# Performance work log

Hardware: AMD Instinct MI355X
Metric: run time of the kernel (lower is better)

The kernel has to match this reference:

```python
import jax, jax.numpy as jnp
import numpy as np

B, T1, T2, D = 16, 64, 64, 1024
PROJ = D // 2


def setup_inputs() -> dict:
    key = jax.random.key(0)
    k1, k2, k3 = jax.random.split(key, 3)
    x = jax.random.normal(k1, (B, T1, T2, D), dtype=jnp.float32)
    # glorot-style scale for params
    W_proj = jax.random.normal(k2, (D, PROJ), dtype=jnp.float32) * (2.0 / (D + PROJ)) ** 0.5
    v_score = jax.random.normal(k3, (PROJ,), dtype=jnp.float32) * (1.0 / PROJ) ** 0.5
    return {"x": x, "W_proj": W_proj, "v_score": v_score}


def reference(x, W_proj, v_score):
    # proj_input = tanh(tensordot(x, W_proj, axes=(3,0)))  -> (B, T1, T2, PROJ)
    proj = jnp.tanh(jnp.einsum('btsd,dp->btsp', x, W_proj))
    # att_scores = tensordot(proj, v_score, axes=(3,0))    -> (B, T1, T2)
    scores = jnp.einsum('btsp,p->bts', proj, v_score)
    # softmax over last axis (T2), weighted sum of x over T2 -> (B, T1, D)
    attn = jax.nn.softmax(scores, axis=-1)
    out = jnp.einsum('bts,btsd->btd', attn, x)
    return out
```

## Files before the change

kernel.cpp:

```cpp
#include <hip/hip_runtime.h>
#include <hip/hip_bf16.h>
#include <math.h>

#define B_    16
#define T1_   64
#define T2_   64
#define D_    1024
#define PROJ_ 512
#define BM    64
#define BK    32
#define NT    (D_ / BK)
#define LDP   40

typedef __attribute__((ext_vector_type(8))) short bf16x8;
typedef __attribute__((ext_vector_type(4))) float f32x4;
typedef __attribute__((ext_vector_type(4))) unsigned int u32x4;

__device__ __forceinline__ unsigned short f2bf(float f) {
  unsigned int u = __builtin_bit_cast(unsigned int, f);
  u += 0x7FFFu + ((u >> 16) & 1u);
  return (unsigned short)(u >> 16);
}

__device__ __forceinline__ float fast_tanh(float a) {
  float t = __builtin_amdgcn_exp2f(a * 2.885390081777927f);
  return 1.0f - 2.0f * __builtin_amdgcn_rcpf(t + 1.0f);
}

__global__ __launch_bounds__(256) void make_bfrag(
    const float* __restrict__ W, unsigned short* __restrict__ wt) {
  __shared__ float tile[32][33];
  const int t  = blockIdx.x;
  const int np = blockIdx.y;
  const int tx = threadIdx.x & 31;
  const int ty = threadIdx.x >> 5;
#pragma unroll
  for (int i = 0; i < 4; ++i)
    tile[ty + i * 8][tx] =
        W[(size_t)(t * 32 + ty + i * 8) * PROJ_ + np * 32 + tx];
  __syncthreads();
  if (threadIdx.x < 128) {
    const int sub  = threadIdx.x >> 6;
    const int lane = threadIdx.x & 63;
    const int llo = lane & 15, lhi = lane >> 4;
    unsigned short o[8];
#pragma unroll
    for (int j = 0; j < 8; ++j)
      o[j] = f2bf(tile[lhi * 8 + j][sub * 16 + llo]);
    const int n16 = np * 2 + sub;
    *(u32x4*)(wt + ((size_t)(t * 32 + n16) * 64 + lane) * 8) = *(const u32x4*)o;
  }
}

__global__ __launch_bounds__(512, 4) void fused_kernel(
    const float* __restrict__ x, const unsigned short* __restrict__ wt,
    const float* __restrict__ v, float* __restrict__ out) {
  __shared__ unsigned short As[2][BM][LDP];
  __shared__ float sp[BM][9];
  __shared__ float attn[BM];
  __shared__ f32x4 xred[256];

  const int tid  = threadIdx.x;
  const int lane = tid & 63;
  const int wid  = tid >> 6;
  const int llo  = lane & 15, lhi = lane >> 4;
  const int bt   = blockIdx.x;
  const int m0   = bt * BM;

  f32x4 acc[4][4];
#pragma unroll
  for (int mf = 0; mf < 4; ++mf)
#pragma unroll
    for (int nf = 0; nf < 4; ++nf) acc[mf][nf] = (f32x4){0.f, 0.f, 0.f, 0.f};

  const int arow = tid >> 3, akc = (tid & 7) * 4;
  const float* asrc = x + (size_t)(m0 + arow) * D_ + akc;

  const u32x4* wt4 = (const u32x4*)wt;
  const int bbase = (wid * 4) * 64 + lane;

  float4 s0 = *(const float4*)(asrc);
  float4 s1 = *(const float4*)(asrc + BK);
  u32x4 rb[4];
#pragma unroll
  for (int nf = 0; nf < 4; ++nf) rb[nf] = wt4[bbase + nf * 64];
  {
    ushort4 ua = {f2bf(s0.x), f2bf(s0.y), f2bf(s0.z), f2bf(s0.w)};
    *(ushort4*)&As[0][arow][akc] = ua;
  }
  asm volatile("s_waitcnt lgkmcnt(0)" ::: "memory");
  __builtin_amdgcn_s_barrier();

#define KSTEP(T, SLD, SCV, BR, BW)                                           \
  {                                                                          \
    bf16x8 af0 = *(const bf16x8*)&As[BR][ 0 + llo][lhi * 8];                 \
    bf16x8 af1 = *(const bf16x8*)&As[BR][16 + llo][lhi * 8];                 \
    bf16x8 af2 = *(const bf16x8*)&As[BR][32 + llo][lhi * 8];                 \
    bf16x8 af3 = *(const bf16x8*)&As[BR][48 + llo][lhi * 8];                 \
    if ((T) + 2 < NT) SLD = *(const float4*)(asrc + ((T) + 2) * BK);         \
    _Pragma("unroll")                                                        \
    for (int nf = 0; nf < 4; ++nf) {                                         \
      bf16x8 bfr = *(const bf16x8*)&rb[nf];                                  \
      acc[0][nf] = __builtin_amdgcn_mfma_f32_16x16x32_bf16(af0, bfr, acc[0][nf], 0, 0, 0); \
      acc[1][nf] = __builtin_amdgcn_mfma_f32_16x16x32_bf16(af1, bfr, acc[1][nf], 0, 0, 0); \
      acc[2][nf] = __builtin_amdgcn_mfma_f32_16x16x32_bf16(af2, bfr, acc[2][nf], 0, 0, 0); \
      acc[3][nf] = __builtin_amdgcn_mfma_f32_16x16x32_bf16(af3, bfr, acc[3][nf], 0, 0, 0); \
      if ((T) + 1 < NT) rb[nf] = wt4[bbase + ((T) + 1) * 2048 + nf * 64];    \
    }                                                                        \
    if ((T) + 1 < NT) {                                                      \
      ushort4 ua = {f2bf(SCV.x), f2bf(SCV.y), f2bf(SCV.z), f2bf(SCV.w)};     \
      *(ushort4*)&As[BW][arow][akc] = ua;                                    \
    }                                                                        \
    asm volatile("s_waitcnt lgkmcnt(0)" ::: "memory");                       \
    __builtin_amdgcn_s_barrier();                                            \
  }

  for (int t = 0; t < NT; t += 2) {
    KSTEP(t,     s0, s1, 0, 1)
    KSTEP(t + 1, s1, s0, 1, 0)
  }
#undef KSTEP

  float vv0 = v[wid * 64 +  0 + llo];
  float vv1 = v[wid * 64 + 16 + llo];
  float vv2 = v[wid * 64 + 32 + llo];
  float vv3 = v[wid * 64 + 48 + llo];
#pragma unroll
  for (int mf = 0; mf < 4; ++mf) {
    float pr[4] = {0.f, 0.f, 0.f, 0.f};
#pragma unroll
    for (int r = 0; r < 4; ++r) {
      pr[r] += fast_tanh(acc[mf][0][r]) * vv0;
      pr[r] += fast_tanh(acc[mf][1][r]) * vv1;
      pr[r] += fast_tanh(acc[mf][2][r]) * vv2;
      pr[r] += fast_tanh(acc[mf][3][r]) * vv3;
    }
#pragma unroll
    for (int r = 0; r < 4; ++r) {
      float p = pr[r];
      p += __shfl_xor(p, 1, 64);
      p += __shfl_xor(p, 2, 64);
      p += __shfl_xor(p, 4, 64);
      p += __shfl_xor(p, 8, 64);
      if (llo == 0) sp[mf * 16 + lhi * 4 + r][wid] = p;
    }
  }
  __syncthreads();

  if (tid < BM) {
    float s = 0.f;
#pragma unroll
    for (int w = 0; w < 8; ++w) s += sp[tid][w];
    float mx = s;
#pragma unroll
    for (int mask = 1; mask < 64; mask <<= 1)
      mx = fmaxf(mx, __shfl_xor(mx, mask, 64));
    const float e = __builtin_amdgcn_exp2f((s - mx) * 1.442695040888963f);
    float sum = e;
#pragma unroll
    for (int mask = 1; mask < 64; mask <<= 1)
      sum += __shfl_xor(sum, mask, 64);
    attn[tid] = e * __builtin_amdgcn_rcpf(sum);
  }
  __syncthreads();

  const int c4 = tid & 255;
  const int sh = tid >> 8;
  const float* xg = x + ((size_t)m0 + sh * 32) * D_ + c4 * 4;
  f32x4 o0 = {0.f,0.f,0.f,0.f}, o1 = o0, o2 = o0, o3 = o0;
#pragma unroll
  for (int s = 0; s < 32; s += 4) {
    const float w0 = attn[sh * 32 + s + 0];
    const float w1 = attn[sh * 32 + s + 1];
    const float w2 = attn[sh * 32 + s + 2];
    const float w3 = attn[sh * 32 + s + 3];
    const float4 a0 = *(const float4*)(xg + (size_t)(s + 0) * D_);
    const float4 a1 = *(const float4*)(xg + (size_t)(s + 1) * D_);
    const float4 a2 = *(const float4*)(xg + (size_t)(s + 2) * D_);
    const float4 a3 = *(const float4*)(xg + (size_t)(s + 3) * D_);
    o0[0] += w0 * a0.x; o0[1] += w0 * a0.y; o0[2] += w0 * a0.z; o0[3] += w0 * a0.w;
    o1[0] += w1 * a1.x; o1[1] += w1 * a1.y; o1[2] += w1 * a1.z; o1[3] += w1 * a1.w;
    o2[0] += w2 * a2.x; o2[1] += w2 * a2.y; o2[2] += w2 * a2.z; o2[3] += w2 * a2.w;
    o3[0] += w3 * a3.x; o3[1] += w3 * a3.y; o3[2] += w3 * a3.z; o3[3] += w3 * a3.w;
  }
  f32x4 o;
#pragma unroll
  for (int j = 0; j < 4; ++j) o[j] = (o0[j] + o1[j]) + (o2[j] + o3[j]);
  if (sh == 1) xred[c4] = o;
  __syncthreads();
  if (sh == 0) {
    f32x4 o2b = xred[c4];
    float4 res = {o[0] + o2b[0], o[1] + o2b[1], o[2] + o2b[2], o[3] + o2b[3]};
    *(float4*)(out + (size_t)bt * D_ + c4 * 4) = res;
  }
}

extern "C" void kernel_launch(void* const* d_in, const int* in_sizes, int n_in,
                              void* d_out, int out_size, void* d_ws, size_t ws_size,
                              hipStream_t stream) {
  const float* x = (const float*)d_in[0];
  const float* W = (const float*)d_in[1];
  const float* v = (const float*)d_in[2];
  float* out = (float*)d_out;
  unsigned short* Wt = (unsigned short*)d_ws;

  make_bfrag<<<dim3(NT, PROJ_ / 32), 256, 0, stream>>>(W, Wt);
  fused_kernel<<<B_ * T1_, 512, 0, stream>>>(x, Wt, v, out);
}
```

Before: 118.9 us.

## Stage weight fragments through LDS via direct global-to-LDS loads

Replaces per-wave register prefetch of the bf16 weight fragments with global_load_lds DMA into a double-buffered LDS region, which each wave then reads back for its MFMA B operand. This is meant to cut register pressure and let the hardware write loaded data straight to LDS, overlapping the next tile's fetch with compute. In exchange it uses about 74KB of LDS per block, which limits how many 512-thread blocks fit per CU. It also adds a full vmcnt(0) wait before every barrier, which stalls on the x prefetch as well.

```diff
diff --git a/kernel.cpp b/kernel.cpp
--- a/kernel.cpp
+++ b/kernel.cpp
@@ -27,6 +27,12 @@
   return 1.0f - 2.0f * __builtin_amdgcn_rcpf(t + 1.0f);
 }
 
+__device__ __forceinline__ void load_lds16(const void* g, void* l) {
+  __builtin_amdgcn_global_load_lds(
+      (const __attribute__((address_space(1))) unsigned int*)g,
+      (__attribute__((address_space(3))) unsigned int*)l, 16, 0, 0);
+}
+
 __global__ __launch_bounds__(256) void make_bfrag(
     const float* __restrict__ W, unsigned short* __restrict__ wt) {
   __shared__ float tile[32][33];
@@ -55,10 +61,14 @@
 __global__ __launch_bounds__(512, 4) void fused_kernel(
     const float* __restrict__ x, const unsigned short* __restrict__ wt,
     const float* __restrict__ v, float* __restrict__ out) {
-  __shared__ unsigned short As[2][BM][LDP];
-  __shared__ float sp[BM][9];
-  __shared__ float attn[BM];
-  __shared__ f32x4 xred[256];
+  __shared__ __align__(16) char smem[75776];
+  unsigned short (*As)[BM][LDP] = (unsigned short(*)[BM][LDP])smem;
+  unsigned short* Bs0 = (unsigned short*)(smem + 10240);
+  unsigned short* Bs1 = Bs0 + 16384;
+#define BSP(i) ((i) ? Bs1 : Bs0)
+  float (*sp)[9] = (float(*)[9])smem;
+  float* attn    = (float*)(smem + 2304);
+  f32x4* xred    = (f32x4*)(smem + 2560);
 
   const int tid  = threadIdx.x;
   const int lane = tid & 63;
@@ -75,43 +85,50 @@
 
   const int arow = tid >> 3, akc = (tid & 7) * 4;
   const float* asrc = x + (size_t)(m0 + arow) * D_ + akc;
-
   const u32x4* wt4 = (const u32x4*)wt;
-  const int bbase = (wid * 4) * 64 + lane;
 
   float4 s0 = *(const float4*)(asrc);
   float4 s1 = *(const float4*)(asrc + BK);
-  u32x4 rb[4];
-#pragma unroll
-  for (int nf = 0; nf < 4; ++nf) rb[nf] = wt4[bbase + nf * 64];
   {
     ushort4 ua = {f2bf(s0.x), f2bf(s0.y), f2bf(s0.z), f2bf(s0.w)};
     *(ushort4*)&As[0][arow][akc] = ua;
   }
-  asm volatile("s_waitcnt lgkmcnt(0)" ::: "memory");
+#pragma unroll
+  for (int c = 0; c < 4; ++c) {
+    const int n16 = c * 8 + wid;
+    load_lds16(wt4 + (size_t)n16 * 64 + lane, Bs0 + n16 * 512);
+  }
+  asm volatile("s_waitcnt vmcnt(0) lgkmcnt(0)" ::: "memory");
   __builtin_amdgcn_s_barrier();
 
 #define KSTEP(T, SLD, SCV, BR, BW)                                           \
   {                                                                          \
+    if ((T) + 1 < NT) {                                                      \
+      _Pragma("unroll")                                                      \
+      for (int c = 0; c < 4; ++c) {                                          \
+        const int n16 = c * 8 + wid;                                         \
+        load_lds16(wt4 + (size_t)(((T) + 1) * 32 + n16) * 64 + lane,         \
+                   BSP(BW) + n16 * 512);                                     \
+      }                                                                      \
+    }                                                                        \
+    if ((T) + 2 < NT) SLD = *(const float4*)(asrc + ((T) + 2) * BK);         \
     bf16x8 af0 = *(const bf16x8*)&As[BR][ 0 + llo][lhi * 8];                 \
     bf16x8 af1 = *(const bf16x8*)&As[BR][16 + llo][lhi * 8];                 \
     bf16x8 af2 = *(const bf16x8*)&As[BR][32 + llo][lhi * 8];                 \
     bf16x8 af3 = *(const bf16x8*)&As[BR][48 + llo][lhi * 8];                 \
-    if ((T) + 2 < NT) SLD = *(const float4*)(asrc + ((T) + 2) * BK);         \
     _Pragma("unroll")                                                        \
     for (int nf = 0; nf < 4; ++nf) {                                         \
-      bf16x8 bfr = *(const bf16x8*)&rb[nf];                                  \
+      bf16x8 bfr = *(const bf16x8*)(BSP(BR) + ((wid * 4 + nf) * 64 + lane) * 8); \
       acc[0][nf] = __builtin_amdgcn_mfma_f32_16x16x32_bf16(af0, bfr, acc[0][nf], 0, 0, 0); \
       acc[1][nf] = __builtin_amdgcn_mfma_f32_16x16x32_bf16(af1, bfr, acc[1][nf], 0, 0, 0); \
       acc[2][nf] = __builtin_amdgcn_mfma_f32_16x16x32_bf16(af2, bfr, acc[2][nf], 0, 0, 0); \
       acc[3][nf] = __builtin_amdgcn_mfma_f32_16x16x32_bf16(af3, bfr, acc[3][nf], 0, 0, 0); \
-      if ((T) + 1 < NT) rb[nf] = wt4[bbase + ((T) + 1) * 2048 + nf * 64];    \
     }                                                                        \
     if ((T) + 1 < NT) {                                                      \
       ushort4 ua = {f2bf(SCV.x), f2bf(SCV.y), f2bf(SCV.z), f2bf(SCV.w)};     \
       *(ushort4*)&As[BW][arow][akc] = ua;                                    \
     }                                                                        \
-    asm volatile("s_waitcnt lgkmcnt(0)" ::: "memory");                       \
+    asm volatile("s_waitcnt vmcnt(0) lgkmcnt(0)" ::: "memory");              \
     __builtin_amdgcn_s_barrier();                                            \
   }
 
@@ -120,6 +137,7 @@
     KSTEP(t + 1, s1, s0, 1, 0)
   }
 #undef KSTEP
+#undef BSP
 
   float vv0 = v[wid * 64 +  0 + llo];
   float vv1 = v[wid * 64 + 16 + llo];
```

Result: slower. 122.5 us (+3.1%).

## Halve block size, loop each wave over two projection slices

Applied to the files above, without the earlier changes.

Shrinks the fused block from 8 waves to 4 and has each wave compute two PROJ slices in sequential passes, restaging the x tile each pass with wider 8-element loads. Adds s_setprio around the MFMA burst and simplifies the final weighted sum so each thread reduces all 64 rows, removing the shared-memory cross-half reduction. The goal is better occupancy and less barrier overhead, at the cost of re-reading and reconverting the x tile twice per block.

```diff
diff --git a/kernel.cpp b/kernel.cpp
--- a/kernel.cpp
+++ b/kernel.cpp
@@ -10,11 +10,14 @@
 #define BM    64
 #define BK    32
 #define NT    (D_ / BK)
+#define NPASS 2
 #define LDP   40
 
 typedef __attribute__((ext_vector_type(8))) short bf16x8;
 typedef __attribute__((ext_vector_type(4))) float f32x4;
 typedef __attribute__((ext_vector_type(4))) unsigned int u32x4;
+
+struct A8 { float4 a, b; };
 
 __device__ __forceinline__ unsigned short f2bf(float f) {
   unsigned int u = __builtin_bit_cast(unsigned int, f);
@@ -52,13 +55,12 @@
   }
 }
 
-__global__ __launch_bounds__(512, 4) void fused_kernel(
+__global__ __launch_bounds__(256, 4) void fused_kernel(
     const float* __restrict__ x, const unsigned short* __restrict__ wt,
     const float* __restrict__ v, float* __restrict__ out) {
   __shared__ unsigned short As[2][BM][LDP];
-  __shared__ float sp[BM][9];
+  __shared__ float sp[BM][8];
   __shared__ float attn[BM];
-  __shared__ f32x4 xred[256];
 
   const int tid  = threadIdx.x;
   const int lane = tid & 63;
@@ -67,29 +69,37 @@
   const int bt   = blockIdx.x;
   const int m0   = bt * BM;
 
-  f32x4 acc[4][4];
-#pragma unroll
-  for (int mf = 0; mf < 4; ++mf)
-#pragma unroll
-    for (int nf = 0; nf < 4; ++nf) acc[mf][nf] = (f32x4){0.f, 0.f, 0.f, 0.f};
-
-  const int arow = tid >> 3, akc = (tid & 7) * 4;
+  const int arow = tid >> 2, akc = (tid & 3) * 8;
   const float* asrc = x + (size_t)(m0 + arow) * D_ + akc;
-
   const u32x4* wt4 = (const u32x4*)wt;
-  const int bbase = (wid * 4) * 64 + lane;
-
-  float4 s0 = *(const float4*)(asrc);
-  float4 s1 = *(const float4*)(asrc + BK);
-  u32x4 rb[4];
-#pragma unroll
-  for (int nf = 0; nf < 4; ++nf) rb[nf] = wt4[bbase + nf * 64];
-  {
-    ushort4 ua = {f2bf(s0.x), f2bf(s0.y), f2bf(s0.z), f2bf(s0.w)};
-    *(ushort4*)&As[0][arow][akc] = ua;
-  }
-  asm volatile("s_waitcnt lgkmcnt(0)" ::: "memory");
-  __builtin_amdgcn_s_barrier();
+
+  for (int p = 0; p < NPASS; ++p) {
+    const int slice = p * 4 + wid;
+    const int bbase = (slice * 4) * 64 + lane;
+
+    f32x4 acc[4][4];
+#pragma unroll
+    for (int mf = 0; mf < 4; ++mf)
+#pragma unroll
+      for (int nf = 0; nf < 4; ++nf) acc[mf][nf] = (f32x4){0.f, 0.f, 0.f, 0.f};
+
+    __syncthreads();
+
+    A8 s0, s1;
+    s0.a = *(const float4*)(asrc);
+    s0.b = *(const float4*)(asrc + 4);
+    s1.a = *(const float4*)(asrc + BK);
+    s1.b = *(const float4*)(asrc + BK + 4);
+    u32x4 rb[4];
+#pragma unroll
+    for (int nf = 0; nf < 4; ++nf) rb[nf] = wt4[bbase + nf * 64];
+    {
+      unsigned short o[8] = {f2bf(s0.a.x), f2bf(s0.a.y), f2bf(s0.a.z), f2bf(s0.a.w),
+                             f2bf(s0.b.x), f2bf(s0.b.y), f2bf(s0.b.z), f2bf(s0.b.w)};
+      *(u32x4*)&As[0][arow][akc] = *(const u32x4*)o;
+    }
+    asm volatile("s_waitcnt lgkmcnt(0)" ::: "memory");
+    __builtin_amdgcn_s_barrier();
 
 #define KSTEP(T, SLD, SCV, BR, BW)                                           \
   {                                                                          \
@@ -97,7 +107,11 @@
     bf16x8 af1 = *(const bf16x8*)&As[BR][16 + llo][lhi * 8];                 \
     bf16x8 af2 = *(const bf16x8*)&As[BR][32 + llo][lhi * 8];                 \
     bf16x8 af3 = *(const bf16x8*)&As[BR][48 + llo][lhi * 8];                 \
-    if ((T) + 2 < NT) SLD = *(const float4*)(asrc + ((T) + 2) * BK);         \
+    if ((T) + 2 < NT) {                                                      \
+      SLD.a = *(const float4*)(asrc + ((T) + 2) * BK);                       \
+      SLD.b = *(const float4*)(asrc + ((T) + 2) * BK + 4);                   \
+    }                                                                        \
+    __builtin_amdgcn_s_setprio(1);                                           \
     _Pragma("unroll")                                                        \
     for (int nf = 0; nf < 4; ++nf) {                                         \
       bf16x8 bfr = *(const bf16x8*)&rb[nf];                                  \
@@ -107,42 +121,47 @@
       acc[3][nf] = __builtin_amdgcn_mfma_f32_16x16x32_bf16(af3, bfr, acc[3][nf], 0, 0, 0); \
       if ((T) + 1 < NT) rb[nf] = wt4[bbase + ((T) + 1) * 2048 + nf * 64];    \
     }                                                                        \
+    __builtin_amdgcn_s_setprio(0);                                           \
     if ((T) + 1 < NT) {                                                      \
-      ushort4 ua = {f2bf(SCV.x), f2bf(SCV.y), f2bf(SCV.z), f2bf(SCV.w)};     \
-      *(ushort4*)&As[BW][arow][akc] = ua;                                    \
+      unsigned short o[8] = {f2bf(SCV.a.x), f2bf(SCV.a.y), f2bf(SCV.a.z), f2bf(SCV.a.w), \
+                             f2bf(SCV.b.x), f2bf(SCV.b.y), f2bf(SCV.b.z), f2bf(SCV.b.w)}; \
+      *(u32x4*)&As[BW][arow][akc] = *(const u32x4*)o;                        \
     }                                                                        \
     asm volatile("s_waitcnt lgkmcnt(0)" ::: "memory");                       \
     __builtin_amdgcn_s_barrier();                                            \
   }
 
-  for (int t = 0; t < NT; t += 2) {
-    KSTEP(t,     s0, s1, 0, 1)
-    KSTEP(t + 1, s1, s0, 1, 0)
-  }
+    for (int t = 0; t < NT; t += 2) {
+      KSTEP(t,     s0, s1, 0, 1)
+      KSTEP(t + 1, s1, s0, 1, 0)
+    }
 #undef KSTEP
 
-  float vv0 = v[wid * 64 +  0 + llo];
-  float vv1 = v[wid * 64 + 16 + llo];
-  float vv2 = v[wid * 64 + 32 + llo];
-  float vv3 = v[wid * 64 + 48 + llo];
-#pragma unroll
-  for (int mf = 0; mf < 4; ++mf) {
-    float pr[4] = {0.f, 0.f, 0.f, 0.f};
-#pragma unroll
-    for (int r = 0; r < 4; ++r) {
-      pr[r] += fast_tanh(acc[mf][0][r]) * vv0;
-      pr[r] += fast_tanh(acc[mf][1][r]) * vv1;
-      pr[r] += fast_tanh(acc[mf][2][r]) * vv2;
-      pr[r] += fast_tanh(acc[mf][3][r]) * vv3;
-    }
-#pragma unroll
-    for (int r = 0; r < 4; ++r) {
-      float p = pr[r];
-      p += __shfl_xor(p, 1, 64);
-      p += __shfl_xor(p, 2, 64);
-      p += __shfl_xor(p, 4, 64);
-      p += __shfl_xor(p, 8, 64);
-      if (llo == 0) sp[mf * 16 + lhi * 4 + r][wid] = p;
+    {
+      const float vv0 = v[slice * 64 +  0 + llo];
+      const float vv1 = v[slice * 64 + 16 + llo];
+      const float vv2 = v[slice * 64 + 32 + llo];
+      const float vv3 = v[slice * 64 + 48 + llo];
+#pragma unroll
+      for (int mf = 0; mf < 4; ++mf) {
+        float pr[4] = {0.f, 0.f, 0.f, 0.f};
+#pragma unroll
+        for (int r = 0; r < 4; ++r) {
+          pr[r] += fast_tanh(acc[mf][0][r]) * vv0;
+          pr[r] += fast_tanh(acc[mf][1][r]) * vv1;
+          pr[r] += fast_tanh(acc[mf][2][r]) * vv2;
+          pr[r] += fast_tanh(acc[mf][3][r]) * vv3;
+        }
+#pragma unroll
+        for (int r = 0; r < 4; ++r) {
+          float pp = pr[r];
+          pp += __shfl_xor(pp, 1, 64);
+          pp += __shfl_xor(pp, 2, 64);
+          pp += __shfl_xor(pp, 4, 64);
+          pp += __shfl_xor(pp, 8, 64);
+          if (llo == 0) sp[mf * 16 + lhi * 4 + r][slice] = pp;
+        }
+      }
     }
   }
   __syncthreads();
@@ -150,7 +169,7 @@
   if (tid < BM) {
     float s = 0.f;
 #pragma unroll
-    for (int w = 0; w < 8; ++w) s += sp[tid][w];
+    for (int sl = 0; sl < 8; ++sl) s += sp[tid][sl];
     float mx = s;
 #pragma unroll
     for (int mask = 1; mask < 64; mask <<= 1)
@@ -164,16 +183,14 @@
   }
   __syncthreads();
 
-  const int c4 = tid & 255;
-  const int sh = tid >> 8;
-  const float* xg = x + ((size_t)m0 + sh * 32) * D_ + c4 * 4;
+  const float* xg = x + (size_t)m0 * D_ + tid * 4;
   f32x4 o0 = {0.f,0.f,0.f,0.f}, o1 = o0, o2 = o0, o3 = o0;
-#pragma unroll
-  for (int s = 0; s < 32; s += 4) {
-    const float w0 = attn[sh * 32 + s + 0];
-    const float w1 = attn[sh * 32 + s + 1];
-    const float w2 = attn[sh * 32 + s + 2];
-    const float w3 = attn[sh * 32 + s + 3];
+#pragma unroll 4
+  for (int s = 0; s < T2_; s += 4) {
+    const float w0 = attn[s + 0];
+    const float w1 = attn[s + 1];
+    const float w2 = attn[s + 2];
+    const float w3 = attn[s + 3];
     const float4 a0 = *(const float4*)(xg + (size_t)(s + 0) * D_);
     const float4 a1 = *(const float4*)(xg + (size_t)(s + 1) * D_);
     const float4 a2 = *(const float4*)(xg + (size_t)(s + 2) * D_);
@@ -183,16 +200,11 @@
     o2[0] += w2 * a2.x; o2[1] += w2 * a2.y; o2[2] += w2 * a2.z; o2[3] += w2 * a2.w;
     o3[0] += w3 * a3.x; o3[1] += w3 * a3.y; o3[2] += w3 * a3.z; o3[3] += w3 * a3.w;
   }
-  f32x4 o;
-#pragma unroll
-  for (int j = 0; j < 4; ++j) o[j] = (o0[j] + o1[j]) + (o2[j] + o3[j]);
-  if (sh == 1) xred[c4] = o;
-  __syncthreads();
-  if (sh == 0) {
-    f32x4 o2b = xred[c4];
-    float4 res = {o[0] + o2b[0], o[1] + o2b[1], o[2] + o2b[2], o[3] + o2b[3]};
-    *(float4*)(out + (size_t)bt * D_ + c4 * 4) = res;
-  }
+  float4 res = {(o0[0] + o1[0]) + (o2[0] + o3[0]),
+                (o0[1] + o1[1]) + (o2[1] + o3[1]),
+                (o0[2] + o1[2]) + (o2[2] + o3[2]),
+                (o0[3] + o1[3]) + (o2[3] + o3[3])};
+  *(float4*)(out + (size_t)bt * D_ + tid * 4) = res;
 }
 
 extern "C" void kernel_launch(void* const* d_in, const int* in_sizes, int n_in,
@@ -205,5 +217,5 @@
   unsigned short* Wt = (unsigned short*)d_ws;
 
   make_bfrag<<<dim3(NT, PROJ_ / 32), 256, 0, stream>>>(W, Wt);
-  fused_kernel<<<B_ * T1_, 512, 0, stream>>>(x, Wt, v, out);
-}
+  fused_kernel<<<B_ * T1_, 256, 0, stream>>>(x, Wt, v, out);
+}
```

Result: slower. 156.8 us (+31.8%).

## Widen A staging to 128-wide K chunks with XOR-swizzled LDS and fewer barriers

Applied to the files above, without the earlier changes.

Each stage now converts and stages a 64x128 bf16 A tile into a double-buffered, XOR-swizzled shared buffer, so the loop runs 8 iterations with 4 MFMA sub-steps each instead of 32 steps with a barrier after every one. The swizzle is meant to avoid LDS bank conflicts on the wider row stride. s_setprio is raised around the MFMA bursts. B fragments are still prefetched one 32-wide K step ahead. Shared memory grows to 32 KB per block, which may reduce occupancy, and larger register staging (16 floats per thread) adds register pressure.

```diff
diff --git a/kernel.cpp b/kernel.cpp
--- a/kernel.cpp
+++ b/kernel.cpp
@@ -8,9 +8,9 @@
 #define D_    1024
 #define PROJ_ 512
 #define BM    64
-#define BK    32
-#define NT    (D_ / BK)
-#define LDP   40
+#define BKS   128
+#define NTS   (D_ / BKS)
+#define ABUF  16384
 
 typedef __attribute__((ext_vector_type(8))) short bf16x8;
 typedef __attribute__((ext_vector_type(4))) float f32x4;
@@ -55,10 +55,10 @@
 __global__ __launch_bounds__(512, 4) void fused_kernel(
     const float* __restrict__ x, const unsigned short* __restrict__ wt,
     const float* __restrict__ v, float* __restrict__ out) {
-  __shared__ unsigned short As[2][BM][LDP];
-  __shared__ float sp[BM][9];
-  __shared__ float attn[BM];
-  __shared__ f32x4 xred[256];
+  __shared__ __align__(16) char smem[2 * ABUF];
+  float (*sp)[9] = (float(*)[9])smem;
+  float* attn    = (float*)(smem + 2304);
+  f32x4* xred    = (f32x4*)(smem + 2560);
 
   const int tid  = threadIdx.x;
   const int lane = tid & 63;
@@ -73,76 +73,106 @@
 #pragma unroll
     for (int nf = 0; nf < 4; ++nf) acc[mf][nf] = (f32x4){0.f, 0.f, 0.f, 0.f};
 
-  const int arow = tid >> 3, akc = (tid & 7) * 4;
+  const int arow = tid >> 3, akc = (tid & 7) * 16;
   const float* asrc = x + (size_t)(m0 + arow) * D_ + akc;
+  const int wb0 = (arow * 256 + akc * 2)        ^ ((arow & 7) << 4);
+  const int wb1 = (arow * 256 + akc * 2 + 16)   ^ ((arow & 7) << 4);
 
   const u32x4* wt4 = (const u32x4*)wt;
   const int bbase = (wid * 4) * 64 + lane;
 
-  float4 s0 = *(const float4*)(asrc);
-  float4 s1 = *(const float4*)(asrc + BK);
+  {
+    float4 p0 = *(const float4*)(asrc);
+    float4 p1 = *(const float4*)(asrc + 4);
+    float4 p2 = *(const float4*)(asrc + 8);
+    float4 p3 = *(const float4*)(asrc + 12);
+    unsigned short o[16] = {f2bf(p0.x), f2bf(p0.y), f2bf(p0.z), f2bf(p0.w),
+                            f2bf(p1.x), f2bf(p1.y), f2bf(p1.z), f2bf(p1.w),
+                            f2bf(p2.x), f2bf(p2.y), f2bf(p2.z), f2bf(p2.w),
+                            f2bf(p3.x), f2bf(p3.y), f2bf(p3.z), f2bf(p3.w)};
+    *(u32x4*)(smem + wb0) = *(const u32x4*)&o[0];
+    *(u32x4*)(smem + wb1) = *(const u32x4*)&o[8];
+  }
   u32x4 rb[4];
 #pragma unroll
   for (int nf = 0; nf < 4; ++nf) rb[nf] = wt4[bbase + nf * 64];
-  {
-    ushort4 ua = {f2bf(s0.x), f2bf(s0.y), f2bf(s0.z), f2bf(s0.w)};
-    *(ushort4*)&As[0][arow][akc] = ua;
-  }
   asm volatile("s_waitcnt lgkmcnt(0)" ::: "memory");
   __builtin_amdgcn_s_barrier();
 
-#define KSTEP(T, SLD, SCV, BR, BW)                                           \
-  {                                                                          \
-    bf16x8 af0 = *(const bf16x8*)&As[BR][ 0 + llo][lhi * 8];                 \
-    bf16x8 af1 = *(const bf16x8*)&As[BR][16 + llo][lhi * 8];                 \
-    bf16x8 af2 = *(const bf16x8*)&As[BR][32 + llo][lhi * 8];                 \
-    bf16x8 af3 = *(const bf16x8*)&As[BR][48 + llo][lhi * 8];                 \
-    if ((T) + 2 < NT) SLD = *(const float4*)(asrc + ((T) + 2) * BK);         \
-    _Pragma("unroll")                                                        \
-    for (int nf = 0; nf < 4; ++nf) {                                         \
-      bf16x8 bfr = *(const bf16x8*)&rb[nf];                                  \
-      acc[0][nf] = __builtin_amdgcn_mfma_f32_16x16x32_bf16(af0, bfr, acc[0][nf], 0, 0, 0); \
-      acc[1][nf] = __builtin_amdgcn_mfma_f32_16x16x32_bf16(af1, bfr, acc[1][nf], 0, 0, 0); \
-      acc[2][nf] = __builtin_amdgcn_mfma_f32_16x16x32_bf16(af2, bfr, acc[2][nf], 0, 0, 0); \
-      acc[3][nf] = __builtin_amdgcn_mfma_f32_16x16x32_bf16(af3, bfr, acc[3][nf], 0, 0, 0); \
-      if ((T) + 1 < NT) rb[nf] = wt4[bbase + ((T) + 1) * 2048 + nf * 64];    \
-    }                                                                        \
-    if ((T) + 1 < NT) {                                                      \
-      ushort4 ua = {f2bf(SCV.x), f2bf(SCV.y), f2bf(SCV.z), f2bf(SCV.w)};     \
-      *(ushort4*)&As[BW][arow][akc] = ua;                                    \
-    }                                                                        \
-    asm volatile("s_waitcnt lgkmcnt(0)" ::: "memory");                       \
-    __builtin_amdgcn_s_barrier();                                            \
-  }
-
-  for (int t = 0; t < NT; t += 2) {
-    KSTEP(t,     s0, s1, 0, 1)
-    KSTEP(t + 1, s1, s0, 1, 0)
-  }
-#undef KSTEP
-
-  float vv0 = v[wid * 64 +  0 + llo];
-  float vv1 = v[wid * 64 + 16 + llo];
-  float vv2 = v[wid * 64 + 32 + llo];
-  float vv3 = v[wid * 64 + 48 + llo];
-#pragma unroll
-  for (int mf = 0; mf < 4; ++mf) {
-    float pr[4] = {0.f, 0.f, 0.f, 0.f};
-#pragma unroll
-    for (int r = 0; r < 4; ++r) {
-      pr[r] += fast_tanh(acc[mf][0][r]) * vv0;
-      pr[r] += fast_tanh(acc[mf][1][r]) * vv1;
-      pr[r] += fast_tanh(acc[mf][2][r]) * vv2;
-      pr[r] += fast_tanh(acc[mf][3][r]) * vv3;
-    }
-#pragma unroll
-    for (int r = 0; r < 4; ++r) {
-      float p = pr[r];
-      p += __shfl_xor(p, 1, 64);
-      p += __shfl_xor(p, 2, 64);
-      p += __shfl_xor(p, 4, 64);
-      p += __shfl_xor(p, 8, 64);
-      if (llo == 0) sp[mf * 16 + lhi * 4 + r][wid] = p;
+  for (int T = 0; T < NTS; ++T) {
+    char* asr = smem + (T & 1) * ABUF;
+    float4 sa0, sa1, sa2, sa3;
+    if (T + 1 < NTS) {
+      const float* p = asrc + (T + 1) * BKS;
+      sa0 = *(const float4*)(p);
+      sa1 = *(const float4*)(p + 4);
+      sa2 = *(const float4*)(p + 8);
+      sa3 = *(const float4*)(p + 12);
+    }
+#pragma unroll
+    for (int ss = 0; ss < 4; ++ss) {
+      const int t32 = T * 4 + ss;
+      __builtin_amdgcn_s_setprio(1);
+#pragma unroll
+      for (int mf = 0; mf < 3; ++mf) {
+        const int row = mf * 16 + llo;
+        bf16x8 af = *(const bf16x8*)(
+            asr + ((row * 256 + (ss * 32 + lhi * 8) * 2) ^ ((row & 7) << 4)));
+        acc[mf][0] = __builtin_amdgcn_mfma_f32_16x16x32_bf16(af, *(const bf16x8*)&rb[0], acc[mf][0], 0, 0, 0);
+        acc[mf][1] = __builtin_amdgcn_mfma_f32_16x16x32_bf16(af, *(const bf16x8*)&rb[1], acc[mf][1], 0, 0, 0);
+        acc[mf][2] = __builtin_amdgcn_mfma_f32_16x16x32_bf16(af, *(const bf16x8*)&rb[2], acc[mf][2], 0, 0, 0);
+        acc[mf][3] = __builtin_amdgcn_mfma_f32_16x16x32_bf16(af, *(const bf16x8*)&rb[3], acc[mf][3], 0, 0, 0);
+      }
+      {
+        const int row = 48 + llo;
+        bf16x8 af = *(const bf16x8*)(
+            asr + ((row * 256 + (ss * 32 + lhi * 8) * 2) ^ ((row & 7) << 4)));
+#pragma unroll
+        for (int nf = 0; nf < 4; ++nf) {
+          acc[3][nf] = __builtin_amdgcn_mfma_f32_16x16x32_bf16(af, *(const bf16x8*)&rb[nf], acc[3][nf], 0, 0, 0);
+          if (t32 + 1 < 32)
+            rb[nf] = wt4[(size_t)(t32 + 1) * 2048 + bbase + nf * 64];
+        }
+      }
+      __builtin_amdgcn_s_setprio(0);
+    }
+    if (T + 1 < NTS) {
+      char* asw = smem + ((T + 1) & 1) * ABUF;
+      unsigned short o[16] = {f2bf(sa0.x), f2bf(sa0.y), f2bf(sa0.z), f2bf(sa0.w),
+                              f2bf(sa1.x), f2bf(sa1.y), f2bf(sa1.z), f2bf(sa1.w),
+                              f2bf(sa2.x), f2bf(sa2.y), f2bf(sa2.z), f2bf(sa2.w),
+                              f2bf(sa3.x), f2bf(sa3.y), f2bf(sa3.z), f2bf(sa3.w)};
+      *(u32x4*)(asw + wb0) = *(const u32x4*)&o[0];
+      *(u32x4*)(asw + wb1) = *(const u32x4*)&o[8];
+    }
+    asm volatile("s_waitcnt lgkmcnt(0)" ::: "memory");
+    __builtin_amdgcn_s_barrier();
+  }
+
+  {
+    const float vv0 = v[wid * 64 +  0 + llo];
+    const float vv1 = v[wid * 64 + 16 + llo];
+    const float vv2 = v[wid * 64 + 32 + llo];
+    const float vv3 = v[wid * 64 + 48 + llo];
+#pragma unroll
+    for (int mf = 0; mf < 4; ++mf) {
+      float pr[4] = {0.f, 0.f, 0.f, 0.f};
+#pragma unroll
+      for (int r = 0; r < 4; ++r) {
+        pr[r] += fast_tanh(acc[mf][0][r]) * vv0;
+        pr[r] += fast_tanh(acc[mf][1][r]) * vv1;
+        pr[r] += fast_tanh(acc[mf][2][r]) * vv2;
+        pr[r] += fast_tanh(acc[mf][3][r]) * vv3;
+      }
+#pragma unroll
+      for (int r = 0; r < 4; ++r) {
+        float p = pr[r];
+        p += __shfl_xor(p, 1, 64);
+        p += __shfl_xor(p, 2, 64);
+        p += __shfl_xor(p, 4, 64);
+        p += __shfl_xor(p, 8, 64);
+        if (llo == 0) sp[mf * 16 + lhi * 4 + r][wid] = p;
+      }
     }
   }
   __syncthreads();
@@ -204,6 +234,6 @@
   float* out = (float*)d_out;
   unsigned short* Wt = (unsigned short*)d_ws;
 
-  make_bfrag<<<dim3(NT, PROJ_ / 32), 256, 0, stream>>>(W, Wt);
+  make_bfrag<<<dim3(32, PROJ_ / 32), 256, 0, stream>>>(W, Wt);
   fused_kernel<<<B_ * T1_, 512, 0, stream>>>(x, Wt, v, out);
 }
```

Measured after the change: 210.4 us. 1.77x slower.
